# Kernel tuning notes

Measured on AMD Instinct MI355X. Metric: run time of the kernel, lower is better.

The kernel has to match this reference:

```python
import jax, jax.numpy as jnp
import numpy as np

NUM_GRAPHS = 64
NEG_SLOPE = 0.2


def _gatv2_conv(x, src, dst, Wl, bl, Wr, br, att, bias):
    # PyG GATv2Conv (concat=True, share_weights=False, residual=False)
    N = x.shape[0]
    H, C = att.shape
    xl = (x @ Wl.T + bl).reshape(N, H, C)  # source transform
    xr = (x @ Wr.T + br).reshape(N, H, C)  # target transform
    e = jax.nn.leaky_relu(xl[src] + xr[dst], NEG_SLOPE)      # [E,H,C]
    alpha = jnp.einsum('ehc,hc->eh', e, att)                 # [E,H]
    # softmax over incoming edges per target node (numerically stable)
    amax = jax.ops.segment_max(alpha, dst, num_segments=N)   # [N,H]
    amax = jnp.where(jnp.isfinite(amax), amax, 0.0)
    ex = jnp.exp(alpha - amax[dst])
    denom = jax.ops.segment_sum(ex, dst, num_segments=N)
    a = ex / (denom[dst] + 1e-16)                            # [E,H]
    out = jax.ops.segment_sum(xl[src] * a[:, :, None], dst, num_segments=N)  # [N,H,C]
    return out.reshape(N, H * C) + bias


def setup_inputs() -> dict:
    key = jax.random.key(0)
    ks = jax.random.split(key, 20)
    N, E, F_in, hidden, H = 50000, 1600000, 256, 128, 4
    C = hidden // H
    s = 0.05
    inp = {
        'x': jax.random.normal(ks[0], (N, F_in), dtype=jnp.float32),
        'edge_index': jax.random.randint(ks[1], (2, E), 0, N, dtype=jnp.int64),
        'batch': jnp.sort(jax.random.randint(ks[2], (N,), 0, NUM_GRAPHS, dtype=jnp.int64)),
        # layer 1 (in=F_in)
        'Wl1': jax.random.normal(ks[3], (hidden, F_in), dtype=jnp.float32) * s,
        'bl1': jnp.zeros((hidden,), dtype=jnp.float32),
        'Wr1': jax.random.normal(ks[4], (hidden, F_in), dtype=jnp.float32) * s,
        'br1': jnp.zeros((hidden,), dtype=jnp.float32),
        'att1': jax.random.normal(ks[5], (H, C), dtype=jnp.float32) * s,
        'bias1': jnp.zeros((hidden,), dtype=jnp.float32),
        # layer 2 (in=hidden)
        'Wl2': jax.random.normal(ks[6], (hidden, hidden), dtype=jnp.float32) * s,
        'bl2': jnp.zeros((hidden,), dtype=jnp.float32),
        'Wr2': jax.random.normal(ks[7], (hidden, hidden), dtype=jnp.float32) * s,
        'br2': jnp.zeros((hidden,), dtype=jnp.float32),
        'att2': jax.random.normal(ks[8], (H, C), dtype=jnp.float32) * s,
        'bias2': jnp.zeros((hidden,), dtype=jnp.float32),
        # head
        'Wlin': jax.random.normal(ks[9], (1, hidden), dtype=jnp.float32) * s,
        'blin': jnp.zeros((1,), dtype=jnp.float32),
    }
    return inp


def reference(x, edge_index, batch, Wl1, bl1, Wr1, br1, att1, bias1,
              Wl2, bl2, Wr2, br2, att2, bias2, Wlin, blin):
    N = x.shape[0]
    loop = jnp.arange(N, dtype=edge_index.dtype)
    src = jnp.concatenate([edge_index[0], loop])  # add_self_loops=True
    dst = jnp.concatenate([edge_index[1], loop])
    h = _gatv2_conv(x, src, dst, Wl1, bl1, Wr1, br1, att1, bias1)
    h = jax.nn.relu(h)  # norm=Identity, dropout no-op in eval
    h = _gatv2_conv(h, src, dst, Wl2, bl2, Wr2, br2, att2, bias2)
    # global_mean_pool
    sums = jax.ops.segment_sum(h, batch, num_segments=NUM_GRAPHS)
    cnt = jax.ops.segment_sum(jnp.ones((N,), h.dtype), batch, num_segments=NUM_GRAPHS)
    pooled = sums / jnp.maximum(cnt, 1.0)[:, None]
    return pooled @ Wlin.T + blin
```

## Files before the change

### kernel.cpp

```cpp
#include <hip/hip_runtime.h>
#include <hip/hip_fp16.h>
#include <math.h>
#include <stdint.h>

#define EPB 4096
#define NBKT 128

typedef _Float16 f16x8 __attribute__((ext_vector_type(8)));
typedef float f32x4 __attribute__((ext_vector_type(4)));
typedef _Float16 h2 __attribute__((ext_vector_type(2)));

template<int CTRL>
__device__ __forceinline__ float dpp_add(float x) {
    union { float f; int i; } u, v;
    u.f = x;
    v.i = __builtin_amdgcn_update_dpp(0, u.i, CTRL, 0xF, 0xF, true);
    return x + v.f;
}
__device__ __forceinline__ float reduce16(float x) {
    x = dpp_add<0xB1>(x);
    x = dpp_add<0x4E>(x);
    x = dpp_add<0x124>(x);
    x = dpp_add<0x128>(x);
    return x;
}

__global__ void k_wpack(const float* __restrict__ Wl, const float* __restrict__ Wr,
                        _Float16* __restrict__ Wp, int K) {
    int t = blockIdx.x * 256 + threadIdx.x;
    int total = (K / 32) * 16 * 64;
    if (t >= total) return;
    int l = t & 63, ct = (t >> 6) & 15, kt = t >> 10;
    int col = ct * 16 + (l & 15);
    int k0 = kt * 32 + (l >> 4) * 8;
    const float* src = (col < 128) ? (Wl + (size_t)col * K + k0)
                                   : (Wr + (size_t)(col - 128) * K + k0);
    union { _Float16 h[8]; uint4 u; } o;
#pragma unroll
    for (int e = 0; e < 8; ++e) o.h[e] = (_Float16)src[e];
    reinterpret_cast<uint4*>(Wp)[t] = o.u;
}

template<int K, int CVT>
__global__ __launch_bounds__(256) void k_gemm_mfma(
    const void* __restrict__ Xin, const _Float16* __restrict__ Wp,
    const float* __restrict__ bl, const float* __restrict__ br,
    float* __restrict__ Y, int N) {
    __shared__ _Float16 xs[32 * K];
    const int t = threadIdx.x, w = t >> 6, l = t & 63;
    const int row0 = blockIdx.x * 32;
    if (CVT) {
        const float* X = (const float*)Xin;
        for (int cid = t; cid < 32 * (K / 4); cid += 256) {
            int r = cid / (K / 4), c4 = (cid % (K / 4)) * 4;
            int gr = row0 + r;
            float4 v = make_float4(0.f, 0.f, 0.f, 0.f);
            if (gr < N) v = *reinterpret_cast<const float4*>(X + (size_t)gr * K + c4);
            h2 lo = {(_Float16)v.x, (_Float16)v.y};
            h2 hi = {(_Float16)v.z, (_Float16)v.w};
            uint2 pk;
            pk.x = __builtin_bit_cast(uint32_t, lo);
            pk.y = __builtin_bit_cast(uint32_t, hi);
            int ba = (r * K * 2 + c4 * 2) ^ ((r & 7) << 4);
            *reinterpret_cast<uint2*>(reinterpret_cast<char*>(xs) + ba) = pk;
        }
    } else {
        const _Float16* X = (const _Float16*)Xin;
        for (int cid = t; cid < 32 * (K / 8); cid += 256) {
            int r = cid / (K / 8), c8 = (cid % (K / 8)) * 8;
            int gr = row0 + r;
            uint4 v = make_uint4(0u, 0u, 0u, 0u);
            if (gr < N) v = *reinterpret_cast<const uint4*>(X + (size_t)gr * K + c8);
            int ba = (r * K * 2 + c8 * 2) ^ ((r & 7) << 4);
            *reinterpret_cast<uint4*>(reinterpret_cast<char*>(xs) + ba) = v;
        }
    }
    __syncthreads();
    f32x4 acc[2][4];
#pragma unroll
    for (int m = 0; m < 2; ++m)
#pragma unroll
        for (int n = 0; n < 4; ++n) acc[m][n] = (f32x4){0.f, 0.f, 0.f, 0.f};
#pragma unroll
    for (int kt = 0; kt < K / 32; ++kt) {
        f16x8 a[2], b[4];
#pragma unroll
        for (int m = 0; m < 2; ++m) {
            int r = m * 16 + (l & 15);
            int ba = (r * K * 2 + kt * 64 + (l >> 4) * 16) ^ ((r & 7) << 4);
            a[m] = *reinterpret_cast<const f16x8*>(reinterpret_cast<const char*>(xs) + ba);
        }
#pragma unroll
        for (int n = 0; n < 4; ++n) {
            int ct = w * 4 + n;
            b[n] = *reinterpret_cast<const f16x8*>(Wp + ((size_t)(kt * 16 + ct) * 64 + l) * 8);
        }
#pragma unroll
        for (int m = 0; m < 2; ++m)
#pragma unroll
            for (int n = 0; n < 4; ++n)
                acc[m][n] = __builtin_amdgcn_mfma_f32_16x16x32_f16(a[m], b[n], acc[m][n], 0, 0, 0);
    }
#pragma unroll
    for (int n = 0; n < 4; ++n) {
        int col = (w * 4 + n) * 16 + (l & 15);
        float bv = (col < 128) ? bl[col] : br[col - 128];
#pragma unroll
        for (int m = 0; m < 2; ++m)
#pragma unroll
            for (int r4 = 0; r4 < 4; ++r4) {
                int gr = row0 + m * 16 + (l >> 4) * 4 + r4;
                if (gr < N) Y[(size_t)gr * 256 + col] = acc[m][n][r4] + bv;
            }
    }
}

__global__ __launch_bounds__(256) void k_hist(const int* __restrict__ dstArr,
                                              int* __restrict__ g_hist, int E) {
    __shared__ int h[NBKT];
    int t = threadIdx.x;
    if (t < NBKT) h[t] = 0;
    __syncthreads();
    int s0 = blockIdx.x * EPB, s1 = min(E, s0 + EPB);
    for (int i = s0 + t; i < s1; i += 256) atomicAdd(&h[dstArr[i] >> 9], 1);
    __syncthreads();
    if (t < NBKT) g_hist[blockIdx.x * NBKT + t] = h[t];
}
__global__ __launch_bounds__(512) void k_part_scan(const int* __restrict__ g_hist,
                                                   int* __restrict__ g_base,
                                                   int* __restrict__ bstart_out,
                                                   int NB1, int E) {
    __shared__ int csum[4][NBKT];
    __shared__ int btot[NBKT];
    __shared__ int bstart[NBKT];
    int tid = threadIdx.x, c = tid >> 7, b = tid & (NBKT - 1);
    int chunk = (NB1 + 3) >> 2;
    int i0 = c * chunk, i1 = min(NB1, i0 + chunk);
    int run = 0;
    for (int i = i0; i < i1; ++i) run += g_hist[i * NBKT + b];
    csum[c][b] = run;
    __syncthreads();
    int mytot = 0;
    if (c == 0) {
        mytot = csum[0][b] + csum[1][b] + csum[2][b] + csum[3][b];
        btot[b] = mytot;
    }
    __syncthreads();
    for (int off = 1; off < NBKT; off <<= 1) {
        int add = 0;
        if (c == 0 && b >= off) add = btot[b - off];
        __syncthreads();
        if (c == 0) btot[b] += add;
        __syncthreads();
    }
    if (c == 0) { bstart[b] = btot[b] - mytot; bstart_out[b] = bstart[b]; }
    if (tid == 0) bstart_out[NBKT] = E;
    __syncthreads();
    int base = bstart[b];
    for (int cc = 0; cc < c; ++cc) base += csum[cc][b];
    run = base;
    for (int i = i0; i < i1; ++i) {
        g_base[i * NBKT + b] = run;
        run += g_hist[i * NBKT + b];
    }
}
__global__ __launch_bounds__(256) void k_scatter(const int* __restrict__ ei,
                                                 const int* __restrict__ g_base,
                                                 uint32_t* __restrict__ tmp, int E) {
    __shared__ int off[NBKT];
    int t = threadIdx.x;
    if (t < NBKT) off[t] = g_base[blockIdx.x * NBKT + t];
    __syncthreads();
    int s0 = blockIdx.x * EPB, s1 = min(E, s0 + EPB);
    for (int i = s0 + t; i < s1; i += 256) {
        int s = ei[i], d = ei[E + i];
        int pos = atomicAdd(&off[d >> 9], 1);
        tmp[pos] = ((uint32_t)s << 16) | (uint32_t)d;
    }
}
__global__ __launch_bounds__(256) void k_bucket_csr(
    const uint32_t* __restrict__ tmp, const int* __restrict__ bstart,
    int* __restrict__ rowptr, int* __restrict__ csr, int N, int E) {
    __shared__ int cnt[512];
    __shared__ int fil[512];
    int b = blockIdx.x, t = threadIdx.x;
    int s0 = bstart[b], s1 = bstart[b + 1];
    cnt[t] = 0; cnt[t + 256] = 0;
    __syncthreads();
    for (int i = s0 + t; i < s1; i += 256)
        atomicAdd(&cnt[tmp[i] & 511], 1);
    __syncthreads();
    int c0 = cnt[t], c1 = cnt[t + 256];
    for (int off = 1; off < 512; off <<= 1) {
        int v0 = (t >= off) ? cnt[t - off] : 0;
        int v1 = (t + 256 >= off) ? cnt[t + 256 - off] : 0;
        __syncthreads();
        cnt[t] += v0; cnt[t + 256] += v1;
        __syncthreads();
    }
    int e0 = cnt[t] - c0, e1 = cnt[t + 256] - c1;
    __syncthreads();
    cnt[t] = e0; cnt[t + 256] = e1;
    fil[t] = 1; fil[t + 256] = 1;
    __syncthreads();
    int n0 = b * 512;
#pragma unroll
    for (int k = 0; k < 2; ++k) {
        int ld = t + k * 256, n = n0 + ld;
        if (n < N) {
            int rp = s0 + cnt[ld] + n;
            rowptr[n] = rp;
            csr[rp] = n;
        }
    }
    if (b == 0 && t == 0) rowptr[N] = E + N;
    for (int i = s0 + t; i < s1; i += 256) {
        uint32_t pk = tmp[i];
        int d = (int)(pk & 0xFFFFu), ld = d & 511;
        int slot = atomicAdd(&fil[ld], 1);
        csr[s0 + cnt[ld] + d + slot] = (int)(pk >> 16);
    }
}

__global__ __launch_bounds__(256) void k_prep(
    const float* __restrict__ xlr, const float* __restrict__ att,
    uint32_t* __restrict__ xlh, float* __restrict__ edl, int N) {
    int wid = threadIdx.x >> 6, l = threadIdx.x & 63;
    int n = blockIdx.x * 4 + wid;
    if (n >= N) return;
    float2 xv = *reinterpret_cast<const float2*>(xlr + (size_t)n * 256 + 2 * l);
    float2 av = *reinterpret_cast<const float2*>(att + 2 * l);
    h2 hp = {(_Float16)xv.x, (_Float16)xv.y};
    xlh[(size_t)n * 64 + l] = __builtin_bit_cast(uint32_t, hp);
    float pl = reduce16(fmaf(av.x, xv.x, av.y * xv.y));
    if ((l & 15) == 0) edl[n * 4 + (l >> 4)] = __expf(0.6f * pl);
}

template<int OUT16>
__global__ __launch_bounds__(256) void k_gat_edge(
    const float* __restrict__ xlr, const uint32_t* __restrict__ xlh,
    const float* __restrict__ edl,
    const float* __restrict__ att, const float* __restrict__ bias,
    const int* __restrict__ rowptr, const int* __restrict__ csr,
    void* __restrict__ out, int N) {
    int wid = threadIdx.x >> 6, l = threadIdx.x & 63;
    int n = blockIdx.x * 4 + wid;
    if (n >= N) return;
    float2 xrv = *reinterpret_cast<const float2*>(xlr + (size_t)n * 256 + 128 + 2 * l);
    float2 av  = *reinterpret_cast<const float2*>(att + 2 * l);
    const float xr0 = xrv.x, xr1 = xrv.y;
    const float a04 = av.x * 0.4f, a14 = av.y * 0.4f;
    const uint32_t l4 = (uint32_t)(l << 2);
    const uint32_t h4 = (uint32_t)((l >> 4) << 2);
    const char* xlhc = (const char*)xlh;
    const char* edlc = (const char*)edl;
    float ssum = 0.f, acc0 = 0.f, acc1 = 0.f;
    int beg = rowptr[n], end = rowptr[n + 1];
    int i = beg;
    for (; i + 3 < end; i += 4) {
        uint32_t q[4]; float ev[4];
#pragma unroll
        for (int e = 0; e < 4; ++e) {
            uint32_t s = (uint32_t)csr[i + e];
            q[e]  = *(const uint32_t*)(xlhc + ((s << 8) + l4));
            ev[e] = *(const float*)(edlc + ((s << 4) + h4));
        }
#pragma unroll
        for (int e = 0; e < 4; ++e) {
            h2 A = __builtin_bit_cast(h2, q[e]);
            float A0 = (float)A.x, A1 = (float)A.y;
            float t0 = A0 + xr0;
            float t1 = A1 + xr1;
            float p = fabsf(t0) * a04;
            p = fmaf(fabsf(t1), a14, p);
            p = reduce16(p);
            float wgt = ev[e] * __expf(p);
            ssum += wgt;
            acc0 = fmaf(wgt, A0, acc0);
            acc1 = fmaf(wgt, A1, acc1);
        }
    }
    for (; i < end; ++i) {
        uint32_t s = (uint32_t)csr[i];
        uint32_t q = *(const uint32_t*)(xlhc + ((s << 8) + l4));
        float ev   = *(const float*)(edlc + ((s << 4) + h4));
        h2 A = __builtin_bit_cast(h2, q);
        float A0 = (float)A.x, A1 = (float)A.y;
        float t0 = A0 + xr0;
        float t1 = A1 + xr1;
        float p = fabsf(t0) * a04;
        p = fmaf(fabsf(t1), a14, p);
        p = reduce16(p);
        float wgt = ev * __expf(p);
        ssum += wgt;
        acc0 = fmaf(wgt, A0, acc0);
        acc1 = fmaf(wgt, A1, acc1);
    }
    float inv = 1.f / ssum;
    float2 bv = *reinterpret_cast<const float2*>(bias + 2 * l);
    float o0 = fmaf(acc0, inv, bv.x);
    float o1 = fmaf(acc1, inv, bv.y);
    if (OUT16) {
        o0 = fmaxf(o0, 0.f); o1 = fmaxf(o1, 0.f);
        h2 oh = {(_Float16)o0, (_Float16)o1};
        ((uint32_t*)out)[(size_t)n * 64 + l] = __builtin_bit_cast(uint32_t, oh);
    } else {
        ((float2*)out)[(size_t)n * 64 + l] = make_float2(o0, o1);
    }
}

__global__ void k_zero(float* __restrict__ p, int n) {
    int i = blockIdx.x * 256 + threadIdx.x;
    if (i < n) p[i] = 0.f;
}
__global__ __launch_bounds__(128) void k_pool(
    const float* __restrict__ h, const int* __restrict__ batch,
    float* __restrict__ pool, float* __restrict__ gcnt, int N) {
    const int NPB = 32;
    int c = threadIdx.x;
    int n0 = blockIdx.x * NPB;
    int n1 = min(n0 + NPB, N);
    float acc = 0.f;
    int curg = -1, cntl = 0;
    for (int n = n0; n < n1; ++n) {
        int g = batch[n];
        if (g != curg) {
            if (curg >= 0) {
                atomicAdd(&pool[curg * 128 + c], acc);
                if (c == 0) atomicAdd(&gcnt[curg], (float)cntl);
            }
            acc = 0.f; cntl = 0; curg = g;
        }
        acc += h[(size_t)n * 128 + c];
        cntl++;
    }
    if (curg >= 0) {
        atomicAdd(&pool[curg * 128 + c], acc);
        if (c == 0) atomicAdd(&gcnt[curg], (float)cntl);
    }
}
__global__ __launch_bounds__(64) void k_head(
    const float* __restrict__ pool, const float* __restrict__ gcnt,
    const float* __restrict__ Wlin, const float* __restrict__ blin,
    float* __restrict__ out, int G) {
    int g = blockIdx.x, l = threadIdx.x;
    float d = pool[g * 128 + l] * Wlin[l] + pool[g * 128 + l + 64] * Wlin[l + 64];
#pragma unroll
    for (int off = 32; off; off >>= 1) d += __shfl_xor(d, off, 64);
    if (l == 0) {
        float cnt = fmaxf(gcnt[g], 1.f);
        out[g] = d / cnt + blin[0];
    }
}

extern "C" void kernel_launch(void* const* d_in, const int* in_sizes, int n_in,
                              void* d_out, int out_size, void* d_ws, size_t ws_size,
                              hipStream_t stream) {
    const float* x     = (const float*)d_in[0];
    const int*   ei    = (const int*)d_in[1];
    const int*   batch = (const int*)d_in[2];
    const float* Wl1   = (const float*)d_in[3];
    const float* bl1   = (const float*)d_in[4];
    const float* Wr1   = (const float*)d_in[5];
    const float* br1   = (const float*)d_in[6];
    const float* att1  = (const float*)d_in[7];
    const float* bias1 = (const float*)d_in[8];
    const float* Wl2   = (const float*)d_in[9];
    const float* bl2   = (const float*)d_in[10];
    const float* Wr2   = (const float*)d_in[11];
    const float* br2   = (const float*)d_in[12];
    const float* att2  = (const float*)d_in[13];
    const float* bias2 = (const float*)d_in[14];
    const float* Wlin  = (const float*)d_in[15];
    const float* blin  = (const float*)d_in[16];

    const int N   = in_sizes[2];
    const int E   = in_sizes[1] / 2;
    const int Fin = in_sizes[0] / N;
    const int G   = out_size;
    (void)n_in; (void)ws_size;

    char* p = (char*)d_ws;
    auto alloc = [&](size_t bytes) -> char* {
        char* r = p;
        p += (bytes + 255) & ~(size_t)255;
        return r;
    };
    float*    xlr   = (float*)alloc((size_t)N * 256 * 4);
    float*    hb    = (float*)alloc((size_t)N * 128 * 4);
    uint32_t* hbh   = (uint32_t*)alloc((size_t)N * 64 * 4);
    float*    wt    = (float*)alloc((size_t)Fin * 256 * 4);
    uint32_t* xlh   = (uint32_t*)alloc((size_t)N * 64 * 4);
    float*    edl   = (float*)alloc((size_t)N * 4 * 4);
    int*      rowptr= (int*)alloc((size_t)(N + 1) * 4);
    int*      csr   = (int*)alloc((size_t)(E + N) * 4);
    float*    poolg = (float*)alloc((size_t)G * 129 * 4);
    float*    pool  = poolg;
    float*    gcnt  = poolg + (size_t)G * 128;

    const int NB1 = (E + EPB - 1) / EPB;
    int*      g_hist = (int*)alloc((size_t)NB1 * NBKT * 4);
    int*      g_base = (int*)alloc((size_t)NB1 * NBKT * 4);
    int*      bstart = (int*)alloc((size_t)(NBKT + 1) * 4);
    uint32_t* tmp = (uint32_t*)xlr;
    _Float16* Wp  = (_Float16*)wt;

    const int wb = (N + 3) / 4;
    const int gb = (N + 31) / 32;

    k_hist<<<NB1, 256, 0, stream>>>(ei + E, g_hist, E);
    k_part_scan<<<1, 512, 0, stream>>>(g_hist, g_base, bstart, NB1, E);
    k_scatter<<<NB1, 256, 0, stream>>>(ei, g_base, tmp, E);
    k_bucket_csr<<<NBKT, 256, 0, stream>>>(tmp, bstart, rowptr, csr, N, E);

    k_wpack<<<((Fin / 32) * 16 * 64 + 255) / 256, 256, 0, stream>>>(Wl1, Wr1, Wp, Fin);
    k_gemm_mfma<256, 1><<<gb, 256, 0, stream>>>(x, Wp, bl1, br1, xlr, N);
    k_prep<<<wb, 256, 0, stream>>>(xlr, att1, xlh, edl, N);
    k_gat_edge<1><<<wb, 256, 0, stream>>>(xlr, xlh, edl, att1, bias1, rowptr, csr, hbh, N);

    k_wpack<<<((128 / 32) * 16 * 64 + 255) / 256, 256, 0, stream>>>(Wl2, Wr2, Wp, 128);
    k_gemm_mfma<128, 0><<<gb, 256, 0, stream>>>(hbh, Wp, bl2, br2, xlr, N);
    k_prep<<<wb, 256, 0, stream>>>(xlr, att2, xlh, edl, N);
    k_gat_edge<0><<<wb, 256, 0, stream>>>(xlr, xlh, edl, att2, bias2, rowptr, csr, hb, N);

    k_zero<<<(G * 129 + 255) / 256, 256, 0, stream>>>(poolg, G * 129);
    k_pool<<<(N + 31) / 32, 128, 0, stream>>>(hb, batch, pool, gcnt, N);
    k_head<<<G, 64, 0, stream>>>(pool, gcnt, Wlin, blin, (float*)d_out, G);
}
```

Baseline: 323.9 us.

## Fuse prep into GEMM epilogue with permuted channel layout

The per-node prep kernel (fp16 packing of xl and per-node exp of the att·xl term) is folded into the MFMA GEMM epilogue. The GEMM now writes packed fp16 xl, a separate float2 xr buffer and edl directly, instead of a full fp32 xl|xr matrix. To make this work, channels are interleaved as (c, c+16) pairs per head. Layer-2 weights are permuted to match, and the edge, pool and head kernels index with the permuted mapping. This removes one kernel launch and a full fp32 write and reread per layer. The cost is more epilogue work and cross-lane reductions inside the GEMM.

Result: faster. 279.5 us (-13.7%).

```diff
diff --git a/kernel.cpp b/kernel.cpp
--- a/kernel.cpp
+++ b/kernel.cpp
@@ -25,6 +25,7 @@
     return x;
 }
 
+template<int PERM>
 __global__ void k_wpack(const float* __restrict__ Wl, const float* __restrict__ Wr,
                         _Float16* __restrict__ Wp, int K) {
     int t = blockIdx.x * 256 + threadIdx.x;
@@ -33,11 +34,19 @@
     int l = t & 63, ct = (t >> 6) & 15, kt = t >> 10;
     int col = ct * 16 + (l & 15);
     int k0 = kt * 32 + (l >> 4) * 8;
-    const float* src = (col < 128) ? (Wl + (size_t)col * K + k0)
-                                   : (Wr + (size_t)(col - 128) * K + k0);
+    const float* src = (col < 128) ? (Wl + (size_t)col * K)
+                                   : (Wr + (size_t)(col - 128) * K);
     union { _Float16 h[8]; uint4 u; } o;
 #pragma unroll
-    for (int e = 0; e < 8; ++e) o.h[e] = (_Float16)src[e];
+    for (int e = 0; e < 8; ++e) {
+        int k = k0 + e, chan;
+        if (PERM) {
+            int m = k >> 1, hh = m >> 4, j = m & 15;
+            int c0 = hh * 32 + j;
+            chan = (k & 1) ? c0 + 16 : c0;
+        } else chan = k;
+        o.h[e] = (_Float16)src[chan];
+    }
     reinterpret_cast<uint4*>(Wp)[t] = o.u;
 }
 
@@ -45,7 +54,9 @@
 __global__ __launch_bounds__(256) void k_gemm_mfma(
     const void* __restrict__ Xin, const _Float16* __restrict__ Wp,
     const float* __restrict__ bl, const float* __restrict__ br,
-    float* __restrict__ Y, int N) {
+    const float* __restrict__ att,
+    uint32_t* __restrict__ xlh, float2* __restrict__ xrp,
+    float* __restrict__ edl, int N) {
     __shared__ _Float16 xs[32 * K];
     const int t = threadIdx.x, w = t >> 6, l = t & 63;
     const int row0 = blockIdx.x * 32;
@@ -101,16 +112,55 @@
             for (int n = 0; n < 4; ++n)
                 acc[m][n] = __builtin_amdgcn_mfma_f32_16x16x32_f16(a[m], b[n], acc[m][n], 0, 0, 0);
     }
-#pragma unroll
-    for (int n = 0; n < 4; ++n) {
-        int col = (w * 4 + n) * 16 + (l & 15);
-        float bv = (col < 128) ? bl[col] : br[col - 128];
+    const int j = l & 15;
+    if (w < 2) {
+        float attv[2][2], bv[2][2];
+#pragma unroll
+        for (int p = 0; p < 2; ++p) {
+            int c0 = (2 * w + p) * 32 + j;
+            attv[p][0] = att[c0]; attv[p][1] = att[c0 + 16];
+            bv[p][0] = bl[c0];    bv[p][1] = bl[c0 + 16];
+        }
 #pragma unroll
         for (int m = 0; m < 2; ++m)
 #pragma unroll
             for (int r4 = 0; r4 < 4; ++r4) {
                 int gr = row0 + m * 16 + (l >> 4) * 4 + r4;
-                if (gr < N) Y[(size_t)gr * 256 + col] = acc[m][n][r4] + bv;
+                bool ok = gr < N;
+#pragma unroll
+                for (int p = 0; p < 2; ++p) {
+                    int h = 2 * w + p;
+                    float v0 = acc[m][2 * p][r4] + bv[p][0];
+                    float v1 = acc[m][2 * p + 1][r4] + bv[p][1];
+                    float part = reduce16(fmaf(attv[p][0], v0, attv[p][1] * v1));
+                    if (ok) {
+                        h2 hp = {(_Float16)v0, (_Float16)v1};
+                        xlh[(size_t)gr * 64 + h * 16 + j] = __builtin_bit_cast(uint32_t, hp);
+                        if (j == 0) edl[gr * 4 + h] = __expf(0.6f * part);
+                    }
+                }
+            }
+    } else {
+        float bv[2][2];
+#pragma unroll
+        for (int p = 0; p < 2; ++p) {
+            int c0 = (2 * (w - 2) + p) * 32 + j;
+            bv[p][0] = br[c0]; bv[p][1] = br[c0 + 16];
+        }
+#pragma unroll
+        for (int m = 0; m < 2; ++m)
+#pragma unroll
+            for (int r4 = 0; r4 < 4; ++r4) {
+                int gr = row0 + m * 16 + (l >> 4) * 4 + r4;
+                if (gr < N) {
+#pragma unroll
+                    for (int p = 0; p < 2; ++p) {
+                        int hh = 2 * (w - 2) + p;
+                        float v0 = acc[m][2 * p][r4] + bv[p][0];
+                        float v1 = acc[m][2 * p + 1][r4] + bv[p][1];
+                        xrp[(size_t)gr * 64 + hh * 16 + j] = make_float2(v0, v1);
+                    }
+                }
             }
     }
 }
@@ -222,57 +272,39 @@
     }
 }
 
-__global__ __launch_bounds__(256) void k_prep(
-    const float* __restrict__ xlr, const float* __restrict__ att,
-    uint32_t* __restrict__ xlh, float* __restrict__ edl, int N) {
-    int wid = threadIdx.x >> 6, l = threadIdx.x & 63;
-    int n = blockIdx.x * 4 + wid;
-    if (n >= N) return;
-    float2 xv = *reinterpret_cast<const float2*>(xlr + (size_t)n * 256 + 2 * l);
-    float2 av = *reinterpret_cast<const float2*>(att + 2 * l);
-    h2 hp = {(_Float16)xv.x, (_Float16)xv.y};
-    xlh[(size_t)n * 64 + l] = __builtin_bit_cast(uint32_t, hp);
-    float pl = reduce16(fmaf(av.x, xv.x, av.y * xv.y));
-    if ((l & 15) == 0) edl[n * 4 + (l >> 4)] = __expf(0.6f * pl);
-}
-
 template<int OUT16>
 __global__ __launch_bounds__(256) void k_gat_edge(
-    const float* __restrict__ xlr, const uint32_t* __restrict__ xlh,
-    const float* __restrict__ edl,
-    const float* __restrict__ att, const float* __restrict__ bias,
+    const uint32_t* __restrict__ xlh, const float2* __restrict__ xrp,
+    const float* __restrict__ edl, const float* __restrict__ att,
+    const float* __restrict__ bias,
     const int* __restrict__ rowptr, const int* __restrict__ csr,
     void* __restrict__ out, int N) {
-    int wid = threadIdx.x >> 6, l = threadIdx.x & 63;
-    int n = blockIdx.x * 4 + wid;
+    const int l = threadIdx.x & 63;
+    const int n = __builtin_amdgcn_readfirstlane(blockIdx.x * 4 + (threadIdx.x >> 6));
     if (n >= N) return;
-    float2 xrv = *reinterpret_cast<const float2*>(xlr + (size_t)n * 256 + 128 + 2 * l);
-    float2 av  = *reinterpret_cast<const float2*>(att + 2 * l);
-    const float xr0 = xrv.x, xr1 = xrv.y;
-    const float a04 = av.x * 0.4f, a14 = av.y * 0.4f;
-    const uint32_t l4 = (uint32_t)(l << 2);
-    const uint32_t h4 = (uint32_t)((l >> 4) << 2);
-    const char* xlhc = (const char*)xlh;
-    const char* edlc = (const char*)edl;
+    const int h = l >> 4, j = l & 15;
+    const int c0 = h * 32 + j, c1 = c0 + 16;
+    const float2 xr = xrp[(size_t)n * 64 + l];
+    const float a04 = att[c0] * 0.4f, a14 = att[c1] * 0.4f;
     float ssum = 0.f, acc0 = 0.f, acc1 = 0.f;
-    int beg = rowptr[n], end = rowptr[n + 1];
+    const int beg = rowptr[n], end = rowptr[n + 1];
     int i = beg;
     for (; i + 3 < end; i += 4) {
+        int sv[4];
+#pragma unroll
+        for (int e = 0; e < 4; ++e) sv[e] = csr[i + e];
         uint32_t q[4]; float ev[4];
 #pragma unroll
         for (int e = 0; e < 4; ++e) {
-            uint32_t s = (uint32_t)csr[i + e];
-            q[e]  = *(const uint32_t*)(xlhc + ((s << 8) + l4));
-            ev[e] = *(const float*)(edlc + ((s << 4) + h4));
+            q[e]  = xlh[(size_t)sv[e] * 64 + l];
+            ev[e] = edl[sv[e] * 4 + h];
         }
 #pragma unroll
         for (int e = 0; e < 4; ++e) {
             h2 A = __builtin_bit_cast(h2, q[e]);
             float A0 = (float)A.x, A1 = (float)A.y;
-            float t0 = A0 + xr0;
-            float t1 = A1 + xr1;
-            float p = fabsf(t0) * a04;
-            p = fmaf(fabsf(t1), a14, p);
+            float p = fabsf(A0 + xr.x) * a04;
+            p = fmaf(fabsf(A1 + xr.y), a14, p);
             p = reduce16(p);
             float wgt = ev[e] * __expf(p);
             ssum += wgt;
@@ -281,15 +313,13 @@
         }
     }
     for (; i < end; ++i) {
-        uint32_t s = (uint32_t)csr[i];
-        uint32_t q = *(const uint32_t*)(xlhc + ((s << 8) + l4));
-        float ev   = *(const float*)(edlc + ((s << 4) + h4));
+        int s = csr[i];
+        uint32_t q = xlh[(size_t)s * 64 + l];
+        float ev = edl[s * 4 + h];
         h2 A = __builtin_bit_cast(h2, q);
         float A0 = (float)A.x, A1 = (float)A.y;
-        float t0 = A0 + xr0;
-        float t1 = A1 + xr1;
-        float p = fabsf(t0) * a04;
-        p = fmaf(fabsf(t1), a14, p);
+        float p = fabsf(A0 + xr.x) * a04;
+        p = fmaf(fabsf(A1 + xr.y), a14, p);
         p = reduce16(p);
         float wgt = ev * __expf(p);
         ssum += wgt;
@@ -297,9 +327,8 @@
         acc1 = fmaf(wgt, A1, acc1);
     }
     float inv = 1.f / ssum;
-    float2 bv = *reinterpret_cast<const float2*>(bias + 2 * l);
-    float o0 = fmaf(acc0, inv, bv.x);
-    float o1 = fmaf(acc1, inv, bv.y);
+    float o0 = fmaf(acc0, inv, bias[c0]);
+    float o1 = fmaf(acc1, inv, bias[c1]);
     if (OUT16) {
         o0 = fmaxf(o0, 0.f); o1 = fmaxf(o1, 0.f);
         h2 oh = {(_Float16)o0, (_Float16)o1};
@@ -344,7 +373,9 @@
     const float* __restrict__ Wlin, const float* __restrict__ blin,
     float* __restrict__ out, int G) {
     int g = blockIdx.x, l = threadIdx.x;
-    float d = pool[g * 128 + l] * Wlin[l] + pool[g * 128 + l + 64] * Wlin[l + 64];
+    float2 pv = ((const float2*)pool)[g * 64 + l];
+    int c0 = (l >> 4) * 32 + (l & 15);
+    float d = pv.x * Wlin[c0] + pv.y * Wlin[c0 + 16];
 #pragma unroll
     for (int off = 32; off; off >>= 1) d += __shfl_xor(d, off, 64);
     if (l == 0) {
@@ -386,12 +417,12 @@
         p += (bytes + 255) & ~(size_t)255;
         return r;
     };
-    float*    xlr   = (float*)alloc((size_t)N * 256 * 4);
-    float*    hb    = (float*)alloc((size_t)N * 128 * 4);
+    uint32_t* xlh   = (uint32_t*)alloc((size_t)N * 64 * 4);
+    float2*   xrp   = (float2*)alloc((size_t)N * 64 * 8);
     uint32_t* hbh   = (uint32_t*)alloc((size_t)N * 64 * 4);
+    float*    hbf   = (float*)alloc((size_t)N * 128 * 4);
+    float*    edl   = (float*)alloc((size_t)N * 4 * 4);
     float*    wt    = (float*)alloc((size_t)Fin * 256 * 4);
-    uint32_t* xlh   = (uint32_t*)alloc((size_t)N * 64 * 4);
-    float*    edl   = (float*)alloc((size_t)N * 4 * 4);
     int*      rowptr= (int*)alloc((size_t)(N + 1) * 4);
     int*      csr   = (int*)alloc((size_t)(E + N) * 4);
     float*    poolg = (float*)alloc((size_t)G * 129 * 4);
@@ -402,7 +433,7 @@
     int*      g_hist = (int*)alloc((size_t)NB1 * NBKT * 4);
     int*      g_base = (int*)alloc((size_t)NB1 * NBKT * 4);
     int*      bstart = (int*)alloc((size_t)(NBKT + 1) * 4);
-    uint32_t* tmp = (uint32_t*)xlr;
+    uint32_t* tmp = (uint32_t*)xrp;
     _Float16* Wp  = (_Float16*)wt;
 
     const int wb = (N + 3) / 4;
@@ -413,17 +444,15 @@
     k_scatter<<<NB1, 256, 0, stream>>>(ei, g_base, tmp, E);
     k_bucket_csr<<<NBKT, 256, 0, stream>>>(tmp, bstart, rowptr, csr, N, E);
 
-    k_wpack<<<((Fin / 32) * 16 * 64 + 255) / 256, 256, 0, stream>>>(Wl1, Wr1, Wp, Fin);
-    k_gemm_mfma<256, 1><<<gb, 256, 0, stream>>>(x, Wp, bl1, br1, xlr, N);
-    k_prep<<<wb, 256, 0, stream>>>(xlr, att1, xlh, edl, N);
-    k_gat_edge<1><<<wb, 256, 0, stream>>>(xlr, xlh, edl, att1, bias1, rowptr, csr, hbh, N);
-
-    k_wpack<<<((128 / 32) * 16 * 64 + 255) / 256, 256, 0, stream>>>(Wl2, Wr2, Wp, 128);
-    k_gemm_mfma<128, 0><<<gb, 256, 0, stream>>>(hbh, Wp, bl2, br2, xlr, N);
-    k_prep<<<wb, 256, 0, stream>>>(xlr, att2, xlh, edl, N);
-    k_gat_edge<0><<<wb, 256, 0, stream>>>(xlr, xlh, edl, att2, bias2, rowptr, csr, hb, N);
+    k_wpack<0><<<((Fin / 32) * 16 * 64 + 255) / 256, 256, 0, stream>>>(Wl1, Wr1, Wp, Fin);
+    k_gemm_mfma<256, 1><<<gb, 256, 0, stream>>>(x, Wp, bl1, br1, att1, xlh, xrp, edl, N);
+    k_gat_edge<1><<<wb, 256, 0, stream>>>(xlh, xrp, edl, att1, bias1, rowptr, csr, hbh, N);
+
+    k_wpack<1><<<((128 / 32) * 16 * 64 + 255) / 256, 256, 0, stream>>>(Wl2, Wr2, Wp, 128);
+    k_gemm_mfma<128, 0><<<gb, 256, 0, stream>>>(hbh, Wp, bl2, br2, att2, xlh, xrp, edl, N);
+    k_gat_edge<0><<<wb, 256, 0, stream>>>(xlh, xrp, edl, att2, bias2, rowptr, csr, hbf, N);
 
     k_zero<<<(G * 129 + 255) / 256, 256, 0, stream>>>(poolg, G * 129);
-    k_pool<<<(N + 31) / 32, 128, 0, stream>>>(hb, batch, pool, gcnt, N);
+    k_pool<<<(N + 31) / 32, 128, 0, stream>>>(hbf, batch, pool, gcnt, N);
     k_head<<<G, 64, 0, stream>>>(pool, gcnt, Wlin, blin, (float*)d_out, G);
 }
```
